# Kernel tuning notes

Hardware: AMD Instinct MI355X
Metric: run time of the kernel (lower is better)

Reference implementation:

```python
import jax, jax.numpy as jnp
import numpy as np

B, S, D, H = 128, 4096, 64, 256  # num_mlps, tokens per MLP, d_model, d_hidden


def setup_inputs() -> dict:
    key = jax.random.key(0)
    kx, k1, k2 = jax.random.split(key, 3)
    x = jax.random.normal(kx, (B, S, D), dtype=jnp.float32)
    # Stacked per-MLP weights (one 2-layer SiLU MLP per batch index, no bias)
    W1 = jax.random.normal(k1, (B, D, H), dtype=jnp.float32) * (1.0 / np.sqrt(D))
    W2 = jax.random.normal(k2, (B, H, D), dtype=jnp.float32) * (1.0 / np.sqrt(H))
    return {"x": x, "W1": W1, "W2": W2}


def reference(x, W1, W2):
    # outputs[i] = mlp_i(x[i]); stacked + residual -> one batched GEMM pair
    h = jax.nn.silu(jnp.einsum('bsd,bdh->bsh', x, W1))  # [B,S,H]
    out = jnp.einsum('bsh,bhd->bsd', h, W2)             # [B,S,D]
    return out + x
```

## Files before the change

### kernel.cpp

```cpp
#include <hip/hip_runtime.h>
#include <stdint.h>

#define BB 128
#define SS 4096
#define DD 64
#define HH 256

typedef short bf16x8 __attribute__((ext_vector_type(8)));
typedef float f32x16 __attribute__((ext_vector_type(16)));
typedef float f32x2 __attribute__((ext_vector_type(2)));

__device__ __forceinline__ uint32_t cvt_pk_bf16(float lo, float hi) {
  uint32_t r;
  asm("v_cvt_pk_bf16_f32 %0, %1, %2" : "=v"(r) : "v"(lo), "v"(hi));
  return r;
}

__device__ __forceinline__ float bflo(uint32_t w) {
  union { uint32_t u; float f; } c; c.u = w << 16; return c.f;
}
__device__ __forceinline__ float bfhi(uint32_t w) {
  union { uint32_t u; float f; } c; c.u = w & 0xffff0000u; return c.f;
}

__device__ __forceinline__ void permswap(uint32_t& a, uint32_t& b) {
  asm("v_permlane32_swap_b32 %0, %1" : "+v"(a), "+v"(b));
}

__device__ __forceinline__ uint32_t silu2_pack(float a, float b) {
  f32x2 v = {a, b};
  f32x2 m = v * (-1.44269504f);
  float ea, eb;
  asm("v_exp_f32 %0, %1" : "=v"(ea) : "v"(m.x));
  asm("v_exp_f32 %0, %1" : "=v"(eb) : "v"(m.y));
  f32x2 d = {ea, eb};
  d = d + (f32x2){1.0f, 1.0f};
  f32x2 r = {__builtin_amdgcn_rcpf(d.x), __builtin_amdgcn_rcpf(d.y)};
  f32x2 o = v * r;
  return cvt_pk_bf16(o.x, o.y);
}

__device__ __forceinline__ void gload16(const void* g, void* l) {
  __builtin_amdgcn_global_load_lds(
      (const __attribute__((address_space(1))) void*)g,
      (__attribute__((address_space(3))) void*)l, 16, 0, 0);
}

__global__ __launch_bounds__(256) void transpose_w(
    const float* __restrict__ W1, const float* __restrict__ W2,
    ushort* __restrict__ W1f, ushort* __restrict__ W2f) {
  int g = blockIdx.x * 256 + threadIdx.x;
  const int half = (BB * DD * HH) / 8;
  float v[8];
  if (g < half) {
    size_t e = (size_t)g * 8;
    int b = (int)(e >> 14);
    int rem = (int)(e & 16383);
    int tile = rem >> 9;
    int lane6 = (rem >> 3) & 63;
    int hc = tile >> 2, kc = tile & 3;
    int h = hc * 32 + (lane6 & 31);
    int d0 = kc * 16 + (lane6 >> 5) * 8;
    const float* src = W1 + ((size_t)b << 14) + h;
#pragma unroll
    for (int j = 0; j < 8; ++j) v[j] = src[(size_t)(d0 + j) << 8];
    uint4 o;
    o.x = cvt_pk_bf16(v[0], v[1]); o.y = cvt_pk_bf16(v[2], v[3]);
    o.z = cvt_pk_bf16(v[4], v[5]); o.w = cvt_pk_bf16(v[6], v[7]);
    *reinterpret_cast<uint4*>(W1f + e) = o;
  } else if (g < 2 * half) {
    size_t e = (size_t)(g - half) * 8;
    int b = (int)(e >> 14);
    int rem = (int)(e & 16383);
    int tile = rem >> 9;
    int lane6 = (rem >> 3) & 63;
    int hc = tile >> 2, mt = (tile >> 1) & 1, c = tile & 1;
    int d = mt * 32 + (lane6 & 31);
    int h0 = hc * 32 + c * 16 + (lane6 >> 5) * 8;
    const float* src = W2 + ((size_t)b << 14) + d;
#pragma unroll
    for (int j = 0; j < 8; ++j) v[j] = src[(size_t)(h0 + j) << 6];
    uint4 o;
    o.x = cvt_pk_bf16(v[0], v[1]); o.y = cvt_pk_bf16(v[2], v[3]);
    o.z = cvt_pk_bf16(v[4], v[5]); o.w = cvt_pk_bf16(v[6], v[7]);
    *reinterpret_cast<uint4*>(W2f + e) = o;
  }
}

__global__ __launch_bounds__(512, 4) void mlp_fused(
    const float* __restrict__ xg, const ushort* __restrict__ w1f,
    const ushort* __restrict__ w2f, float* __restrict__ outg) {
  __shared__ int4 lds4[65536 / 16];
  char* lds = (char*)lds4;

  const int tid = threadIdx.x;
  const int wave = tid >> 6;
  const int lane = tid & 63;
  const int l31 = lane & 31;
  const int g5 = lane >> 5;

  int raw = blockIdx.x;
  int logical = (raw & 7) * 256 + (raw >> 3);
  const int b = logical >> 4;
  const int st = logical & 15;
  const int s_base = st * 256 + wave * 32;

  const char* w1b = (const char*)(w1f + ((size_t)b << 14));
  const char* w2b = (const char*)(w2f + ((size_t)b << 14));
  char* xlds = lds + 32768;

#pragma unroll
  for (int r = 0; r < 4; ++r) {
    uint32_t o = (uint32_t)(r * 8192 + tid * 16);
    gload16(w1b + o, lds + o);
  }

  const float* xblk = xg + (((size_t)b * SS + st * 256) << 6);
#pragma unroll
  for (int ps = 0; ps < 4; ++ps) {
    int e = ps * 4096 + tid * 8;
    float4 fa = *reinterpret_cast<const float4*>(xblk + e);
    float4 fb = *reinterpret_cast<const float4*>(xblk + e + 4);
    uint4 pk;
    pk.x = cvt_pk_bf16(fa.x, fa.y);
    pk.y = cvt_pk_bf16(fa.z, fa.w);
    pk.z = cvt_pk_bf16(fb.x, fb.y);
    pk.w = cvt_pk_bf16(fb.z, fb.w);
    int row = e >> 6, d0 = e & 63;
    uint32_t byte = (uint32_t)(row * 128 + d0 * 2);
    byte ^= (uint32_t)(row & 7) << 4;
    *reinterpret_cast<uint4*>(xlds + byte) = pk;
  }

  __syncthreads();

  const int R = wave * 32 + l31;
  const uint32_t rs = (uint32_t)(R & 7) << 4;

  bf16x8 bx[4];
#pragma unroll
  for (int kc = 0; kc < 4; ++kc) {
    uint32_t byte = (uint32_t)(R * 128 + kc * 32 + g5 * 16) ^ rs;
    bx[kc] = *reinterpret_cast<const bf16x8*>(xlds + byte);
  }

  f32x16 acc[2];
#pragma unroll
  for (int mt = 0; mt < 2; ++mt)
#pragma unroll
    for (int q = 0; q < 4; ++q) {
      uint32_t byte = (uint32_t)(R * 128 + mt * 64 + q * 16 + g5 * 8) ^ rs;
      uint2 w = *reinterpret_cast<const uint2*>(xlds + byte);
      acc[mt][4 * q + 0] = bflo(w.x);
      acc[mt][4 * q + 1] = bfhi(w.x);
      acc[mt][4 * q + 2] = bflo(w.y);
      acc[mt][4 * q + 3] = bfhi(w.y);
    }

  __syncthreads();

#pragma unroll
  for (int r = 0; r < 4; ++r) {
    uint32_t o = (uint32_t)(r * 8192 + tid * 16);
    gload16(w2b + o, xlds + o);
  }

  __syncthreads();

  const char* lw1 = lds + lane * 16;
  const char* lw2 = xlds + lane * 16;

  const f32x16 vzero = {0.f, 0.f, 0.f, 0.f, 0.f, 0.f, 0.f, 0.f,
                        0.f, 0.f, 0.f, 0.f, 0.f, 0.f, 0.f, 0.f};

#pragma unroll
  for (int hc = 0; hc < 8; ++hc) {
    f32x16 ah = vzero;
#pragma unroll
    for (int kc = 0; kc < 4; ++kc) {
      bf16x8 a1 = *reinterpret_cast<const bf16x8*>(lw1 + (hc * 4 + kc) * 1024);
      ah = __builtin_amdgcn_mfma_f32_32x32x16_bf16(a1, bx[kc], ah, 0, 0, 0);
    }

    bf16x8 bh[2];
#pragma unroll
    for (int c = 0; c < 2; ++c) {
      uint32_t A0 = silu2_pack(ah[8 * c + 0], ah[8 * c + 1]);
      uint32_t A1 = silu2_pack(ah[8 * c + 2], ah[8 * c + 3]);
      uint32_t B0 = silu2_pack(ah[8 * c + 4], ah[8 * c + 5]);
      uint32_t B1 = silu2_pack(ah[8 * c + 6], ah[8 * c + 7]);
      permswap(A0, B0);
      permswap(A1, B1);
      union { uint32_t u[4]; bf16x8 v; } f;
      f.u[0] = A0; f.u[1] = A1; f.u[2] = B0; f.u[3] = B1;
      bh[c] = f.v;
    }

#pragma unroll
    for (int c = 0; c < 2; ++c)
#pragma unroll
      for (int mt = 0; mt < 2; ++mt) {
        bf16x8 a2 = *reinterpret_cast<const bf16x8*>(
            lw2 + (hc * 4 + mt * 2 + c) * 1024);
        acc[mt] =
            __builtin_amdgcn_mfma_f32_32x32x16_bf16(a2, bh[c], acc[mt], 0, 0, 0);
      }
  }

  __syncthreads();

  char* slice = lds + wave * 8192;
  {
    uint32_t sw = (uint32_t)(l31 & 7) << 4;
#pragma unroll
    for (int mt = 0; mt < 2; ++mt)
#pragma unroll
      for (int q = 0; q < 4; ++q) {
        uint32_t byte =
            ((uint32_t)(l31 * 256 + mt * 128 + q * 32 + g5 * 16)) ^ sw;
        float4 v;
        v.x = acc[mt][4 * q + 0];
        v.y = acc[mt][4 * q + 1];
        v.z = acc[mt][4 * q + 2];
        v.w = acc[mt][4 * q + 3];
        *reinterpret_cast<float4*>(slice + byte) = v;
      }
  }
  __builtin_amdgcn_sched_barrier(0);
  {
    float* orow = outg + (((size_t)b * SS + s_base) << 6);
#pragma unroll
    for (int it = 0; it < 8; ++it) {
      uint32_t o = (uint32_t)(it * 1024 + lane * 16);
      uint32_t row = o >> 8;
      uint32_t byte = o ^ ((row & 7) << 4);
      float4 v = *reinterpret_cast<const float4*>(slice + byte);
      *reinterpret_cast<float4*>(orow + ((size_t)row << 6) + ((o & 255) >> 2)) =
          v;
    }
  }
}

extern "C" void kernel_launch(void* const* d_in, const int* in_sizes, int n_in,
                              void* d_out, int out_size, void* d_ws, size_t ws_size,
                              hipStream_t stream) {
  const float* x  = (const float*)d_in[0];
  const float* W1 = (const float*)d_in[1];
  const float* W2 = (const float*)d_in[2];
  float* out = (float*)d_out;

  ushort* W1f = (ushort*)d_ws;
  ushort* W2f = W1f + (size_t)BB * DD * HH;

  transpose_w<<<2048, 256, 0, stream>>>(W1, W2, W1f, W2f);
  mlp_fused<<<2048, 512, 0, stream>>>(x, W1f, W2f, out);
}
```

Before: 78.90 us.

## Software-pipeline the first GEMM ahead of the W2 load and second GEMM

The first hidden chunk's GEMM1 and SiLU now run before the barrier that waits for W2 to arrive in LDS, so the W2 load latency is overlapped with compute. The loop is restructured so GEMM2 for chunk hc is followed by GEMM1 and SiLU for chunk hc+1, and the MFMA sections are bracketed with s_setprio so co-resident waves interleave matrix and vector work. The output staging swizzle is widened from 8 to 16 rows to reduce LDS bank conflicts. This adds code duplication and possibly register pressure under the 4-blocks launch bound.

```diff
diff --git a/kernel.cpp b/kernel.cpp
--- a/kernel.cpp
+++ b/kernel.cpp
@@ -165,24 +165,22 @@
     gload16(w2b + o, xlds + o);
   }
 
-  __syncthreads();
-
   const char* lw1 = lds + lane * 16;
   const char* lw2 = xlds + lane * 16;
 
   const f32x16 vzero = {0.f, 0.f, 0.f, 0.f, 0.f, 0.f, 0.f, 0.f,
                         0.f, 0.f, 0.f, 0.f, 0.f, 0.f, 0.f, 0.f};
 
-#pragma unroll
-  for (int hc = 0; hc < 8; ++hc) {
+  bf16x8 bh[2];
+  {
     f32x16 ah = vzero;
+    __builtin_amdgcn_s_setprio(1);
 #pragma unroll
     for (int kc = 0; kc < 4; ++kc) {
-      bf16x8 a1 = *reinterpret_cast<const bf16x8*>(lw1 + (hc * 4 + kc) * 1024);
+      bf16x8 a1 = *reinterpret_cast<const bf16x8*>(lw1 + kc * 1024);
       ah = __builtin_amdgcn_mfma_f32_32x32x16_bf16(a1, bx[kc], ah, 0, 0, 0);
     }
-
-    bf16x8 bh[2];
+    __builtin_amdgcn_s_setprio(0);
 #pragma unroll
     for (int c = 0; c < 2; ++c) {
       uint32_t A0 = silu2_pack(ah[8 * c + 0], ah[8 * c + 1]);
@@ -195,7 +193,13 @@
       f.u[0] = A0; f.u[1] = A1; f.u[2] = B0; f.u[3] = B1;
       bh[c] = f.v;
     }
-
+  }
+
+  __syncthreads();
+
+#pragma unroll
+  for (int hc = 0; hc < 8; ++hc) {
+    __builtin_amdgcn_s_setprio(1);
 #pragma unroll
     for (int c = 0; c < 2; ++c)
 #pragma unroll
@@ -205,13 +209,38 @@
         acc[mt] =
             __builtin_amdgcn_mfma_f32_32x32x16_bf16(a2, bh[c], acc[mt], 0, 0, 0);
       }
+    __builtin_amdgcn_s_setprio(0);
+
+    if (hc < 7) {
+      f32x16 ah = vzero;
+      __builtin_amdgcn_s_setprio(1);
+#pragma unroll
+      for (int kc = 0; kc < 4; ++kc) {
+        bf16x8 a1 = *reinterpret_cast<const bf16x8*>(
+            lw1 + ((hc + 1) * 4 + kc) * 1024);
+        ah = __builtin_amdgcn_mfma_f32_32x32x16_bf16(a1, bx[kc], ah, 0, 0, 0);
+      }
+      __builtin_amdgcn_s_setprio(0);
+#pragma unroll
+      for (int c = 0; c < 2; ++c) {
+        uint32_t A0 = silu2_pack(ah[8 * c + 0], ah[8 * c + 1]);
+        uint32_t A1 = silu2_pack(ah[8 * c + 2], ah[8 * c + 3]);
+        uint32_t B0 = silu2_pack(ah[8 * c + 4], ah[8 * c + 5]);
+        uint32_t B1 = silu2_pack(ah[8 * c + 6], ah[8 * c + 7]);
+        permswap(A0, B0);
+        permswap(A1, B1);
+        union { uint32_t u[4]; bf16x8 v; } f;
+        f.u[0] = A0; f.u[1] = A1; f.u[2] = B0; f.u[3] = B1;
+        bh[c] = f.v;
+      }
+    }
   }
 
   __syncthreads();
 
   char* slice = lds + wave * 8192;
   {
-    uint32_t sw = (uint32_t)(l31 & 7) << 4;
+    uint32_t sw = (uint32_t)(l31 & 15) << 4;
 #pragma unroll
     for (int mt = 0; mt < 2; ++mt)
 #pragma unroll
@@ -233,7 +262,7 @@
     for (int it = 0; it < 8; ++it) {
       uint32_t o = (uint32_t)(it * 1024 + lane * 16);
       uint32_t row = o >> 8;
-      uint32_t byte = o ^ ((row & 7) << 4);
+      uint32_t byte = o ^ ((row & 15) << 4);
       float4 v = *reinterpret_cast<const float4*>(slice + byte);
       *reinterpret_cast<float4*>(orow + ((size_t)row << 6) + ((o & 255) >> 2)) =
           v;
```

Measured after the change: 79.99 us. About the same (+1.4%).

## Process 512 tokens per block with two N-tiles per wave to reuse weights

Applied to the files above, without the earlier changes.

Each block now covers 512 tokens of one MLP instead of 256, so the grid is halved. Each wave computes two 32-row token tiles against the same W1/W2 fragments in LDS, which halves the per-token cost of staging weights and reading weight fragments. The x tile is staged in two halves through the same LDS buffer, with a wider XOR swizzle. The launch-bounds occupancy hint drops from 4 to 3 because the doubled accumulators raise register pressure, and the larger per-block work may hurt latency hiding and tail balance.

```diff
diff --git a/kernel.cpp b/kernel.cpp
--- a/kernel.cpp
+++ b/kernel.cpp
@@ -87,7 +87,7 @@
   }
 }
 
-__global__ __launch_bounds__(512, 4) void mlp_fused(
+__global__ __launch_bounds__(512, 3) void mlp_fused(
     const float* __restrict__ xg, const ushort* __restrict__ w1f,
     const ushort* __restrict__ w2f, float* __restrict__ outg) {
   __shared__ int4 lds4[65536 / 16];
@@ -100,10 +100,9 @@
   const int g5 = lane >> 5;
 
   int raw = blockIdx.x;
-  int logical = (raw & 7) * 256 + (raw >> 3);
-  const int b = logical >> 4;
-  const int st = logical & 15;
-  const int s_base = st * 256 + wave * 32;
+  int logical = (raw & 7) * 128 + (raw >> 3);
+  const int b = logical >> 3;
+  const int st = logical & 7;
 
   const char* w1b = (const char*)(w1f + ((size_t)b << 14));
   const char* w2b = (const char*)(w2f + ((size_t)b << 14));
@@ -115,56 +114,63 @@
     gload16(w1b + o, lds + o);
   }
 
-  const float* xblk = xg + (((size_t)b * SS + st * 256) << 6);
-#pragma unroll
-  for (int ps = 0; ps < 4; ++ps) {
-    int e = ps * 4096 + tid * 8;
-    float4 fa = *reinterpret_cast<const float4*>(xblk + e);
-    float4 fb = *reinterpret_cast<const float4*>(xblk + e + 4);
-    uint4 pk;
-    pk.x = cvt_pk_bf16(fa.x, fa.y);
-    pk.y = cvt_pk_bf16(fa.z, fa.w);
-    pk.z = cvt_pk_bf16(fb.x, fb.y);
-    pk.w = cvt_pk_bf16(fb.z, fb.w);
-    int row = e >> 6, d0 = e & 63;
-    uint32_t byte = (uint32_t)(row * 128 + d0 * 2);
-    byte ^= (uint32_t)(row & 7) << 4;
-    *reinterpret_cast<uint4*>(xlds + byte) = pk;
-  }
-
-  __syncthreads();
-
-  const int R = wave * 32 + l31;
-  const uint32_t rs = (uint32_t)(R & 7) << 4;
-
-  bf16x8 bx[4];
-#pragma unroll
-  for (int kc = 0; kc < 4; ++kc) {
-    uint32_t byte = (uint32_t)(R * 128 + kc * 32 + g5 * 16) ^ rs;
-    bx[kc] = *reinterpret_cast<const bf16x8*>(xlds + byte);
-  }
-
-  f32x16 acc[2];
-#pragma unroll
-  for (int mt = 0; mt < 2; ++mt)
-#pragma unroll
-    for (int q = 0; q < 4; ++q) {
-      uint32_t byte = (uint32_t)(R * 128 + mt * 64 + q * 16 + g5 * 8) ^ rs;
-      uint2 w = *reinterpret_cast<const uint2*>(xlds + byte);
-      acc[mt][4 * q + 0] = bflo(w.x);
-      acc[mt][4 * q + 1] = bfhi(w.x);
-      acc[mt][4 * q + 2] = bflo(w.y);
-      acc[mt][4 * q + 3] = bfhi(w.y);
-    }
-
-  __syncthreads();
+  const float* xblk = xg + (((size_t)b * SS + st * 512) << 6);
+
+  bf16x8 bx[2][4];
+  f32x16 acc[2][2];
+
+#pragma unroll
+  for (int half = 0; half < 2; ++half) {
+    const float* xh = xblk + half * 16384;
+#pragma unroll
+    for (int ps = 0; ps < 4; ++ps) {
+      int e = ps * 4096 + tid * 8;
+      float4 fa = *reinterpret_cast<const float4*>(xh + e);
+      float4 fb = *reinterpret_cast<const float4*>(xh + e + 4);
+      uint4 pk;
+      pk.x = cvt_pk_bf16(fa.x, fa.y);
+      pk.y = cvt_pk_bf16(fa.z, fa.w);
+      pk.z = cvt_pk_bf16(fb.x, fb.y);
+      pk.w = cvt_pk_bf16(fb.z, fb.w);
+      int row = e >> 6, d0 = e & 63;
+      uint32_t byte = (uint32_t)(row * 128 + d0 * 2);
+      byte ^= (uint32_t)(row & 15) << 4;
+      *reinterpret_cast<uint4*>(xlds + byte) = pk;
+    }
+    __syncthreads();
+
+    if ((wave >> 2) == half) {
+#pragma unroll
+      for (int nt = 0; nt < 2; ++nt) {
+        int r = ((wave & 3) * 64 + nt * 32 + l31) & 255;
+        uint32_t rs = (uint32_t)(r & 15) << 4;
+#pragma unroll
+        for (int kc = 0; kc < 4; ++kc) {
+          uint32_t byte = (uint32_t)(r * 128 + kc * 32 + g5 * 16) ^ rs;
+          bx[nt][kc] = *reinterpret_cast<const bf16x8*>(xlds + byte);
+        }
+#pragma unroll
+        for (int mt = 0; mt < 2; ++mt)
+#pragma unroll
+          for (int q = 0; q < 4; ++q) {
+            uint32_t byte =
+                (uint32_t)(r * 128 + mt * 64 + q * 16 + g5 * 8) ^ rs;
+            uint2 w = *reinterpret_cast<const uint2*>(xlds + byte);
+            acc[nt][mt][4 * q + 0] = bflo(w.x);
+            acc[nt][mt][4 * q + 1] = bfhi(w.x);
+            acc[nt][mt][4 * q + 2] = bflo(w.y);
+            acc[nt][mt][4 * q + 3] = bfhi(w.y);
+          }
+      }
+    }
+    __syncthreads();
+  }
 
 #pragma unroll
   for (int r = 0; r < 4; ++r) {
     uint32_t o = (uint32_t)(r * 8192 + tid * 16);
     gload16(w2b + o, xlds + o);
   }
-
   __syncthreads();
 
   const char* lw1 = lds + lane * 16;
@@ -175,25 +181,38 @@
 
 #pragma unroll
   for (int hc = 0; hc < 8; ++hc) {
-    f32x16 ah = vzero;
+    f32x16 ah0 = vzero, ah1 = vzero;
 #pragma unroll
     for (int kc = 0; kc < 4; ++kc) {
       bf16x8 a1 = *reinterpret_cast<const bf16x8*>(lw1 + (hc * 4 + kc) * 1024);
-      ah = __builtin_amdgcn_mfma_f32_32x32x16_bf16(a1, bx[kc], ah, 0, 0, 0);
-    }
-
-    bf16x8 bh[2];
+      ah0 = __builtin_amdgcn_mfma_f32_32x32x16_bf16(a1, bx[0][kc], ah0, 0, 0, 0);
+      ah1 = __builtin_amdgcn_mfma_f32_32x32x16_bf16(a1, bx[1][kc], ah1, 0, 0, 0);
+    }
+
+    bf16x8 bh0[2], bh1[2];
 #pragma unroll
     for (int c = 0; c < 2; ++c) {
-      uint32_t A0 = silu2_pack(ah[8 * c + 0], ah[8 * c + 1]);
-      uint32_t A1 = silu2_pack(ah[8 * c + 2], ah[8 * c + 3]);
-      uint32_t B0 = silu2_pack(ah[8 * c + 4], ah[8 * c + 5]);
-      uint32_t B1 = silu2_pack(ah[8 * c + 6], ah[8 * c + 7]);
+      uint32_t A0 = silu2_pack(ah0[8 * c + 0], ah0[8 * c + 1]);
+      uint32_t A1 = silu2_pack(ah0[8 * c + 2], ah0[8 * c + 3]);
+      uint32_t B0 = silu2_pack(ah0[8 * c + 4], ah0[8 * c + 5]);
+      uint32_t B1 = silu2_pack(ah0[8 * c + 6], ah0[8 * c + 7]);
       permswap(A0, B0);
       permswap(A1, B1);
       union { uint32_t u[4]; bf16x8 v; } f;
       f.u[0] = A0; f.u[1] = A1; f.u[2] = B0; f.u[3] = B1;
-      bh[c] = f.v;
+      bh0[c] = f.v;
+    }
+#pragma unroll
+    for (int c = 0; c < 2; ++c) {
+      uint32_t A0 = silu2_pack(ah1[8 * c + 0], ah1[8 * c + 1]);
+      uint32_t A1 = silu2_pack(ah1[8 * c + 2], ah1[8 * c + 3]);
+      uint32_t B0 = silu2_pack(ah1[8 * c + 4], ah1[8 * c + 5]);
+      uint32_t B1 = silu2_pack(ah1[8 * c + 6], ah1[8 * c + 7]);
+      permswap(A0, B0);
+      permswap(A1, B1);
+      union { uint32_t u[4]; bf16x8 v; } f;
+      f.u[0] = A0; f.u[1] = A1; f.u[2] = B0; f.u[3] = B1;
+      bh1[c] = f.v;
     }
 
 #pragma unroll
@@ -202,16 +221,19 @@
       for (int mt = 0; mt < 2; ++mt) {
         bf16x8 a2 = *reinterpret_cast<const bf16x8*>(
             lw2 + (hc * 4 + mt * 2 + c) * 1024);
-        acc[mt] =
-            __builtin_amdgcn_mfma_f32_32x32x16_bf16(a2, bh[c], acc[mt], 0, 0, 0);
+        acc[0][mt] =
+            __builtin_amdgcn_mfma_f32_32x32x16_bf16(a2, bh0[c], acc[0][mt], 0, 0, 0);
+        acc[1][mt] =
+            __builtin_amdgcn_mfma_f32_32x32x16_bf16(a2, bh1[c], acc[1][mt], 0, 0, 0);
       }
   }
 
   __syncthreads();
 
   char* slice = lds + wave * 8192;
-  {
-    uint32_t sw = (uint32_t)(l31 & 7) << 4;
+#pragma unroll
+  for (int nt = 0; nt < 2; ++nt) {
+    uint32_t sw = (uint32_t)(l31 & 15) << 4;
 #pragma unroll
     for (int mt = 0; mt < 2; ++mt)
 #pragma unroll
@@ -219,25 +241,25 @@
         uint32_t byte =
             ((uint32_t)(l31 * 256 + mt * 128 + q * 32 + g5 * 16)) ^ sw;
         float4 v;
-        v.x = acc[mt][4 * q + 0];
-        v.y = acc[mt][4 * q + 1];
-        v.z = acc[mt][4 * q + 2];
-        v.w = acc[mt][4 * q + 3];
+        v.x = acc[nt][mt][4 * q + 0];
+        v.y = acc[nt][mt][4 * q + 1];
+        v.z = acc[nt][mt][4 * q + 2];
+        v.w = acc[nt][mt][4 * q + 3];
         *reinterpret_cast<float4*>(slice + byte) = v;
       }
-  }
-  __builtin_amdgcn_sched_barrier(0);
-  {
-    float* orow = outg + (((size_t)b * SS + s_base) << 6);
+    __builtin_amdgcn_sched_barrier(0);
+    float* orow =
+        outg + (((size_t)b * SS + st * 512 + wave * 64 + nt * 32) << 6);
 #pragma unroll
     for (int it = 0; it < 8; ++it) {
       uint32_t o = (uint32_t)(it * 1024 + lane * 16);
       uint32_t row = o >> 8;
-      uint32_t byte = o ^ ((row & 7) << 4);
+      uint32_t byte = o ^ ((row & 15) << 4);
       float4 v = *reinterpret_cast<const float4*>(slice + byte);
       *reinterpret_cast<float4*>(orow + ((size_t)row << 6) + ((o & 255) >> 2)) =
           v;
     }
+    __builtin_amdgcn_sched_barrier(0);
   }
 }
 
@@ -253,5 +275,5 @@
   ushort* W2f = W1f + (size_t)BB * DD * HH;
 
   transpose_w<<<2048, 256, 0, stream>>>(W1, W2, W1f, W2f);
-  mlp_fused<<<2048, 512, 0, stream>>>(x, W1f, W2f, out);
-}
+  mlp_fused<<<1024, 512, 0, stream>>>(x, W1f, W2f, out);
+}
```

Result: slower. 99.36 us (+25.9%).

## Shrink LDS footprint to 48KB by staging x, W2, and output in halves

Applied to the files above, without the earlier changes.

Cuts the kernel's shared memory from 64KB to 48KB. x is staged in two halves, with each half-block of waves reading its rows. W2 is loaded in two 16KB phases, with a barrier between the hidden-chunk halves. The output epilogue is also split per mt. The intent is to fit more 512-thread blocks per CU and so hide latency better. In exchange it adds several extra __syncthreads and serialises the W2 load in the middle of compute. The explicit min-blocks hint is also dropped from launch_bounds.

```diff
diff --git a/kernel.cpp b/kernel.cpp
--- a/kernel.cpp
+++ b/kernel.cpp
@@ -87,10 +87,10 @@
   }
 }
 
-__global__ __launch_bounds__(512, 4) void mlp_fused(
+__global__ __launch_bounds__(512) void mlp_fused(
     const float* __restrict__ xg, const ushort* __restrict__ w1f,
     const ushort* __restrict__ w2f, float* __restrict__ outg) {
-  __shared__ int4 lds4[65536 / 16];
+  __shared__ int4 lds4[49152 / 16];
   char* lds = (char*)lds4;
 
   const int tid = threadIdx.x;
@@ -116,55 +116,58 @@
   }
 
   const float* xblk = xg + (((size_t)b * SS + st * 256) << 6);
-#pragma unroll
-  for (int ps = 0; ps < 4; ++ps) {
-    int e = ps * 4096 + tid * 8;
-    float4 fa = *reinterpret_cast<const float4*>(xblk + e);
-    float4 fb = *reinterpret_cast<const float4*>(xblk + e + 4);
-    uint4 pk;
-    pk.x = cvt_pk_bf16(fa.x, fa.y);
-    pk.y = cvt_pk_bf16(fa.z, fa.w);
-    pk.z = cvt_pk_bf16(fb.x, fb.y);
-    pk.w = cvt_pk_bf16(fb.z, fb.w);
-    int row = e >> 6, d0 = e & 63;
-    uint32_t byte = (uint32_t)(row * 128 + d0 * 2);
-    byte ^= (uint32_t)(row & 7) << 4;
-    *reinterpret_cast<uint4*>(xlds + byte) = pk;
-  }
-
-  __syncthreads();
-
-  const int R = wave * 32 + l31;
-  const uint32_t rs = (uint32_t)(R & 7) << 4;
 
   bf16x8 bx[4];
-#pragma unroll
-  for (int kc = 0; kc < 4; ++kc) {
-    uint32_t byte = (uint32_t)(R * 128 + kc * 32 + g5 * 16) ^ rs;
-    bx[kc] = *reinterpret_cast<const bf16x8*>(xlds + byte);
-  }
-
   f32x16 acc[2];
-#pragma unroll
-  for (int mt = 0; mt < 2; ++mt)
-#pragma unroll
-    for (int q = 0; q < 4; ++q) {
-      uint32_t byte = (uint32_t)(R * 128 + mt * 64 + q * 16 + g5 * 8) ^ rs;
-      uint2 w = *reinterpret_cast<const uint2*>(xlds + byte);
-      acc[mt][4 * q + 0] = bflo(w.x);
-      acc[mt][4 * q + 1] = bfhi(w.x);
-      acc[mt][4 * q + 2] = bflo(w.y);
-      acc[mt][4 * q + 3] = bfhi(w.y);
-    }
-
-  __syncthreads();
-
-#pragma unroll
-  for (int r = 0; r < 4; ++r) {
+
+#pragma unroll
+  for (int hf = 0; hf < 2; ++hf) {
+    const float* xh = xblk + hf * 8192;
+#pragma unroll
+    for (int ps = 0; ps < 2; ++ps) {
+      int e = ps * 4096 + tid * 8;
+      float4 fa = *reinterpret_cast<const float4*>(xh + e);
+      float4 fb = *reinterpret_cast<const float4*>(xh + e + 4);
+      uint4 pk;
+      pk.x = cvt_pk_bf16(fa.x, fa.y);
+      pk.y = cvt_pk_bf16(fa.z, fa.w);
+      pk.z = cvt_pk_bf16(fb.x, fb.y);
+      pk.w = cvt_pk_bf16(fb.z, fb.w);
+      int row = e >> 6, d0 = e & 63;
+      uint32_t byte = (uint32_t)(row * 128 + d0 * 2);
+      byte ^= (uint32_t)(row & 7) << 4;
+      *reinterpret_cast<uint4*>(xlds + byte) = pk;
+    }
+    __syncthreads();
+
+    if ((wave >> 2) == hf) {
+      int r = (wave & 3) * 32 + l31;
+      uint32_t rs = (uint32_t)(r & 7) << 4;
+#pragma unroll
+      for (int kc = 0; kc < 4; ++kc) {
+        uint32_t byte = (uint32_t)(r * 128 + kc * 32 + g5 * 16) ^ rs;
+        bx[kc] = *reinterpret_cast<const bf16x8*>(xlds + byte);
+      }
+#pragma unroll
+      for (int mt = 0; mt < 2; ++mt)
+#pragma unroll
+        for (int q = 0; q < 4; ++q) {
+          uint32_t byte = (uint32_t)(r * 128 + mt * 64 + q * 16 + g5 * 8) ^ rs;
+          uint2 w = *reinterpret_cast<const uint2*>(xlds + byte);
+          acc[mt][4 * q + 0] = bflo(w.x);
+          acc[mt][4 * q + 1] = bfhi(w.x);
+          acc[mt][4 * q + 2] = bflo(w.y);
+          acc[mt][4 * q + 3] = bfhi(w.y);
+        }
+    }
+    __syncthreads();
+  }
+
+#pragma unroll
+  for (int r = 0; r < 2; ++r) {
     uint32_t o = (uint32_t)(r * 8192 + tid * 16);
     gload16(w2b + o, xlds + o);
   }
-
   __syncthreads();
 
   const char* lw1 = lds + lane * 16;
@@ -174,70 +177,82 @@
                         0.f, 0.f, 0.f, 0.f, 0.f, 0.f, 0.f, 0.f};
 
 #pragma unroll
-  for (int hc = 0; hc < 8; ++hc) {
-    f32x16 ah = vzero;
-#pragma unroll
-    for (int kc = 0; kc < 4; ++kc) {
-      bf16x8 a1 = *reinterpret_cast<const bf16x8*>(lw1 + (hc * 4 + kc) * 1024);
-      ah = __builtin_amdgcn_mfma_f32_32x32x16_bf16(a1, bx[kc], ah, 0, 0, 0);
-    }
-
-    bf16x8 bh[2];
-#pragma unroll
-    for (int c = 0; c < 2; ++c) {
-      uint32_t A0 = silu2_pack(ah[8 * c + 0], ah[8 * c + 1]);
-      uint32_t A1 = silu2_pack(ah[8 * c + 2], ah[8 * c + 3]);
-      uint32_t B0 = silu2_pack(ah[8 * c + 4], ah[8 * c + 5]);
-      uint32_t B1 = silu2_pack(ah[8 * c + 6], ah[8 * c + 7]);
-      permswap(A0, B0);
-      permswap(A1, B1);
-      union { uint32_t u[4]; bf16x8 v; } f;
-      f.u[0] = A0; f.u[1] = A1; f.u[2] = B0; f.u[3] = B1;
-      bh[c] = f.v;
-    }
-
-#pragma unroll
-    for (int c = 0; c < 2; ++c)
-#pragma unroll
-      for (int mt = 0; mt < 2; ++mt) {
-        bf16x8 a2 = *reinterpret_cast<const bf16x8*>(
-            lw2 + (hc * 4 + mt * 2 + c) * 1024);
-        acc[mt] =
-            __builtin_amdgcn_mfma_f32_32x32x16_bf16(a2, bh[c], acc[mt], 0, 0, 0);
-      }
+  for (int ph = 0; ph < 2; ++ph) {
+#pragma unroll
+    for (int hq = 0; hq < 4; ++hq) {
+      const int hc = ph * 4 + hq;
+      f32x16 ah = vzero;
+#pragma unroll
+      for (int kc = 0; kc < 4; ++kc) {
+        bf16x8 a1 =
+            *reinterpret_cast<const bf16x8*>(lw1 + (hc * 4 + kc) * 1024);
+        ah = __builtin_amdgcn_mfma_f32_32x32x16_bf16(a1, bx[kc], ah, 0, 0, 0);
+      }
+
+      bf16x8 bh[2];
+#pragma unroll
+      for (int c = 0; c < 2; ++c) {
+        uint32_t A0 = silu2_pack(ah[8 * c + 0], ah[8 * c + 1]);
+        uint32_t A1 = silu2_pack(ah[8 * c + 2], ah[8 * c + 3]);
+        uint32_t B0 = silu2_pack(ah[8 * c + 4], ah[8 * c + 5]);
+        uint32_t B1 = silu2_pack(ah[8 * c + 6], ah[8 * c + 7]);
+        permswap(A0, B0);
+        permswap(A1, B1);
+        union { uint32_t u[4]; bf16x8 v; } f;
+        f.u[0] = A0; f.u[1] = A1; f.u[2] = B0; f.u[3] = B1;
+        bh[c] = f.v;
+      }
+
+#pragma unroll
+      for (int c = 0; c < 2; ++c)
+#pragma unroll
+        for (int mt = 0; mt < 2; ++mt) {
+          bf16x8 a2 = *reinterpret_cast<const bf16x8*>(
+              lw2 + (hq * 4 + mt * 2 + c) * 1024);
+          acc[mt] = __builtin_amdgcn_mfma_f32_32x32x16_bf16(a2, bh[c], acc[mt],
+                                                            0, 0, 0);
+        }
+    }
+
+    if (ph == 0) {
+      __syncthreads();
+#pragma unroll
+      for (int r = 0; r < 2; ++r) {
+        uint32_t o = (uint32_t)(r * 8192 + tid * 16);
+        gload16(w2b + 16384 + o, xlds + o);
+      }
+      __syncthreads();
+    }
   }
 
   __syncthreads();
 
-  char* slice = lds + wave * 8192;
-  {
+  char* slice = lds + wave * 4096;
+  float* orow = outg + (((size_t)b * SS + s_base) << 6);
+#pragma unroll
+  for (int mt = 0; mt < 2; ++mt) {
     uint32_t sw = (uint32_t)(l31 & 7) << 4;
 #pragma unroll
-    for (int mt = 0; mt < 2; ++mt)
-#pragma unroll
-      for (int q = 0; q < 4; ++q) {
-        uint32_t byte =
-            ((uint32_t)(l31 * 256 + mt * 128 + q * 32 + g5 * 16)) ^ sw;
-        float4 v;
-        v.x = acc[mt][4 * q + 0];
-        v.y = acc[mt][4 * q + 1];
-        v.z = acc[mt][4 * q + 2];
-        v.w = acc[mt][4 * q + 3];
-        *reinterpret_cast<float4*>(slice + byte) = v;
-      }
-  }
-  __builtin_amdgcn_sched_barrier(0);
-  {
-    float* orow = outg + (((size_t)b * SS + s_base) << 6);
-#pragma unroll
-    for (int it = 0; it < 8; ++it) {
+    for (int q = 0; q < 4; ++q) {
+      uint32_t byte = ((uint32_t)(l31 * 128 + q * 32 + g5 * 16)) ^ sw;
+      float4 v;
+      v.x = acc[mt][4 * q + 0];
+      v.y = acc[mt][4 * q + 1];
+      v.z = acc[mt][4 * q + 2];
+      v.w = acc[mt][4 * q + 3];
+      *reinterpret_cast<float4*>(slice + byte) = v;
+    }
+    __builtin_amdgcn_sched_barrier(0);
+#pragma unroll
+    for (int it = 0; it < 4; ++it) {
       uint32_t o = (uint32_t)(it * 1024 + lane * 16);
-      uint32_t row = o >> 8;
+      uint32_t row = o >> 7;
       uint32_t byte = o ^ ((row & 7) << 4);
       float4 v = *reinterpret_cast<const float4*>(slice + byte);
-      *reinterpret_cast<float4*>(orow + ((size_t)row << 6) + ((o & 255) >> 2)) =
-          v;
-    }
+      *reinterpret_cast<float4*>(orow + ((size_t)row << 6) + mt * 32 +
+                                 ((o & 127) >> 2)) = v;
+    }
+    __builtin_amdgcn_sched_barrier(0);
   }
 }
 
```

Measured after the change: 83.27 us. +5.5%, slower.
